# Kernel tuning notes

Measured on AMD Instinct MI355X. Metric: run time of the kernel, lower is better.

Reference implementation:

```python
import jax, jax.numpy as jnp
import numpy as np
from jax import lax

Q_SCALE = 128.0  # Q1.7 fixed point: 1 sign bit, 7 fractional bits


def quant_comp(x):
    """Q1.7 quantize (floor, clamp to [-128,127]) then force LSB=1 in the
    8-bit two's-complement pattern (equivalent to integer bitwise-or 1),
    then dequantize. Matches quantize_and_compensate_activation."""
    q = jnp.clip(jnp.floor(x * Q_SCALE), -128.0, 127.0).astype(jnp.int32)
    q = jnp.bitwise_or(q, 1)  # set LSB; in-range stays in [-127, 127]
    return q.astype(jnp.float32) / Q_SCALE


def conv2d(x, w, b, pad):
    y = lax.conv_general_dilated(
        x, w, window_strides=(1, 1), padding=[(pad, pad), (pad, pad)],
        dimension_numbers=("NCHW", "OIHW", "NCHW"))
    return y + b[None, :, None, None]


def maxpool2(x):
    return lax.reduce_window(x, -jnp.inf, lax.max,
                             (1, 1, 2, 2), (1, 1, 2, 2), "VALID")


def setup_inputs() -> dict:
    key = jax.random.key(0)
    ks = jax.random.split(key, 12)
    B = 16384

    def u(k, shape, fan_in):
        bound = 1.0 / np.sqrt(fan_in)
        return jax.random.uniform(k, shape, jnp.float32, -bound, bound)

    return {
        "x": jax.random.normal(ks[0], (B, 1, 28, 28), jnp.float32),
        "conv1_w": u(ks[1], (6, 1, 5, 5), 1 * 25),
        "conv1_b": u(ks[2], (6,), 1 * 25),
        "conv2_w": u(ks[3], (16, 6, 5, 5), 6 * 25),
        "conv2_b": u(ks[4], (16,), 6 * 25),
        "fc1_w": u(ks[5], (120, 400), 400),
        "fc1_b": u(ks[6], (120,), 400),
        "fc2_w": u(ks[7], (84, 120), 120),
        "fc2_b": u(ks[8], (84,), 120),
        "fc3_w": u(ks[9], (10, 84), 84),
        "fc3_b": u(ks[10], (10,), 84),
        "quant_act": 1,
    }


def reference(x, conv1_w, conv1_b, conv2_w, conv2_b,
              fc1_w, fc1_b, fc2_w, fc2_b, fc3_w, fc3_b, quant_act):
    q = bool(quant_act)
    if q:
        x = quant_comp(x)
    x = maxpool2(jax.nn.relu(conv2d(x, conv1_w, conv1_b, pad=2)))  # [B,6,14,14]
    if q:
        x = quant_comp(x)
    x = maxpool2(jax.nn.relu(conv2d(x, conv2_w, conv2_b, pad=0)))  # [B,16,5,5]
    if q:
        x = quant_comp(x)
    x = x.reshape(x.shape[0], -1)  # [B,400]
    x = jax.nn.relu(x @ fc1_w.T + fc1_b)
    if q:
        x = quant_comp(x)
    # dropout is identity in eval mode
    x = jax.nn.relu(x @ fc2_w.T + fc2_b)
    if q:
        x = quant_comp(x)
    return x @ fc3_w.T + fc3_b  # [B,10]
```

## Files before the change

kernel.cpp:

```cpp
#include <hip/hip_runtime.h>

#define Q_INV (1.0f / 128.0f)

__device__ __forceinline__ float quant_comp_f(float v) {
    float f = floorf(v * 128.0f);
    f = fminf(fmaxf(f, -128.0f), 127.0f);
    int qi = (int)f;
    qi |= 1;
    return (float)qi * Q_INV;
}

__device__ __forceinline__ float getf(const float4 v, const int c) {
    return c == 0 ? v.x : (c == 1 ? v.y : (c == 2 ? v.z : v.w));
}

__global__ __launch_bounds__(192) void conv_fused_kernel(
    const float* __restrict__ x,
    const float* __restrict__ c1w, const float* __restrict__ c1b,
    const float* __restrict__ c2w, const float* __restrict__ c2b,
    const int* __restrict__ qflag,
    float* __restrict__ act)
{
    __shared__ __align__(16) float shpool[3680];
    __shared__ float w1s[150];
    __shared__ float b1s[6];
    __shared__ float b2s[16];
    __shared__ __align__(16) float mid[6][14][20];

    float (*pin)[36] = reinterpret_cast<float(*)[36]>(shpool);

    const int t = threadIdx.x;
    const int img = blockIdx.x;
    const bool q = (qflag[0] != 0);

    for (int i = t; i < 1152; i += 192) shpool[i] = 0.0f;
    if (t < 150) w1s[t] = c1w[t];
    if (t < 6) b1s[t] = c1b[t];
    if (t < 16) b2s[t] = c2b[t];
    __syncthreads();

    const float* xi = x + (size_t)img * 784;
    for (int i = t; i < 784; i += 192) {
        float v = xi[i];
        if (q) v = quant_comp_f(v);
        pin[i / 28 + 2][i % 28 + 2] = v;
    }
    __syncthreads();

    float hmax1[14];
    if (t < 168) {
        const int c = t / 28, oh = t % 28;
        float acc[28];
        #pragma unroll
        for (int j = 0; j < 28; ++j) acc[j] = 0.0f;
        #pragma unroll
        for (int ky = 0; ky < 5; ++ky) {
            const float4* pr = reinterpret_cast<const float4*>(&pin[oh + ky][0]);
            float4 r4[8];
            #pragma unroll
            for (int j = 0; j < 8; ++j) r4[j] = pr[j];
            #pragma unroll
            for (int kx = 0; kx < 5; ++kx) {
                const float wv = w1s[c * 25 + ky * 5 + kx];
                #pragma unroll
                for (int ow = 0; ow < 28; ++ow) {
                    const int idx = ow + kx;
                    acc[ow] = fmaf(getf(r4[idx >> 2], idx & 3), wv, acc[ow]);
                }
            }
        }
        const float bb = b1s[c];
        #pragma unroll
        for (int j = 0; j < 14; ++j) {
            float v0 = acc[2*j] + bb;
            float v1 = acc[2*j + 1] + bb;
            hmax1[j] = fmaxf(v0, v1);
        }
    }
    __syncthreads();
    if (t < 168) {
        const int c = t / 28, oh = t % 28;
        #pragma unroll
        for (int j = 0; j < 14; ++j) shpool[(c * 28 + oh) * 17 + j] = hmax1[j];
    }
    __syncthreads();
    if (t < 84) {
        const int c = t / 14, ph = t % 14;
        #pragma unroll
        for (int j = 0; j < 14; ++j) {
            float m = fmaxf(shpool[(c * 28 + 2 * ph) * 17 + j],
                            shpool[(c * 28 + 2 * ph + 1) * 17 + j]);
            m = fmaxf(m, 0.0f);
            if (q) m = quant_comp_f(m);
            mid[c][ph][j] = m;
        }
    }
    __syncthreads();

    {
        const float4* src = reinterpret_cast<const float4*>(c2w);
        float4* dst = reinterpret_cast<float4*>(shpool);
        for (int i = t; i < 600; i += 192) dst[i] = src[i];
    }
    __syncthreads();

    const float* w2s = shpool;
    float* rowmax2 = shpool + 2400;

    float hmax2[5];
    if (t < 160) {
        const int c = t / 10, oh = t % 10;
        float acc[10];
        #pragma unroll
        for (int j = 0; j < 10; ++j) acc[j] = 0.0f;
        #pragma unroll
        for (int ky = 0; ky < 5; ++ky) {
            float4 rb4[6][4];
            #pragma unroll
            for (int ic = 0; ic < 6; ++ic) {
                const float4* mr = reinterpret_cast<const float4*>(&mid[ic][oh + ky][0]);
                #pragma unroll
                for (int j2 = 0; j2 < 4; ++j2) rb4[ic][j2] = mr[j2];
            }
            #pragma unroll
            for (int kx = 0; kx < 5; ++kx) {
                #pragma unroll
                for (int ic = 0; ic < 6; ++ic) {
                    const float wv = w2s[(c * 6 + ic) * 25 + ky * 5 + kx];
                    #pragma unroll
                    for (int ow = 0; ow < 10; ++ow) {
                        const int idx = ow + kx;
                        acc[ow] = fmaf(getf(rb4[ic][idx >> 2], idx & 3), wv, acc[ow]);
                    }
                }
            }
        }
        const float bb = b2s[c];
        #pragma unroll
        for (int j = 0; j < 5; ++j) {
            float v0 = acc[2*j] + bb;
            float v1 = acc[2*j + 1] + bb;
            hmax2[j] = fmaxf(v0, v1);
        }
    }
    if (t < 160) {
        const int c = t / 10, oh = t % 10;
        #pragma unroll
        for (int j = 0; j < 5; ++j) rowmax2[(c * 10 + oh) * 8 + j] = hmax2[j];
    }
    __syncthreads();
    if (t < 80) {
        const int c = t / 5, ph = t % 5;
        float* ao = act + (size_t)img * 400;
        #pragma unroll
        for (int j = 0; j < 5; ++j) {
            float m = fmaxf(rowmax2[(c * 10 + 2 * ph) * 8 + j],
                            rowmax2[(c * 10 + 2 * ph + 1) * 8 + j]);
            m = fmaxf(m, 0.0f);
            if (q) m = quant_comp_f(m);
            ao[c * 25 + ph * 5 + j] = m;
        }
    }
}

__global__ __launch_bounds__(256) void fc_fused_kernel(
    const float* __restrict__ act,
    const float* __restrict__ w1, const float* __restrict__ b1,
    const float* __restrict__ w2, const float* __restrict__ b2,
    const float* __restrict__ w3, const float* __restrict__ b3,
    const int* __restrict__ qflag,
    float* __restrict__ out, int B)
{
    __shared__ __align__(16) float wt[120][44];
    __shared__ __align__(16) float a0c[16][44];
    __shared__ __align__(16) float a1[16][124];
    __shared__ __align__(16) float a2[16][88];

    const int t = threadIdx.x;
    const bool q = (qflag[0] != 0);
    const int base = blockIdx.x * 16;
    const int im = t & 15;
    const int grp = t >> 4;

    float acc[8];
    #pragma unroll
    for (int j = 0; j < 8; ++j) acc[j] = 0.0f;

    for (int ch = 0; ch < 10; ++ch) {
        __syncthreads();
        for (int i = t; i < 1200; i += 256) {
            const int o = i / 10, s = i % 10;
            *reinterpret_cast<float4*>(&wt[o][s * 4]) =
                *reinterpret_cast<const float4*>(w1 + o * 400 + ch * 40 + s * 4);
        }
        for (int i = t; i < 640; i += 256) {
            const int imm = i / 40, k = i % 40;
            if (base + imm < B)
                a0c[imm][k] = act[(size_t)(base + imm) * 400 + ch * 40 + k];
        }
        __syncthreads();
        #pragma unroll
        for (int r = 0; r < 4; ++r) {
            const int o0 = r * 32 + 2 * grp;
            if (o0 < 120) {
                float s0 = acc[2*r], s1 = acc[2*r+1];
                #pragma unroll
                for (int kk = 0; kk < 10; ++kk) {
                    const float4 av = *reinterpret_cast<const float4*>(&a0c[im][kk*4]);
                    const float4 wa = *reinterpret_cast<const float4*>(&wt[o0][kk*4]);
                    const float4 wb = *reinterpret_cast<const float4*>(&wt[o0+1][kk*4]);
                    s0 = fmaf(av.x, wa.x, s0); s1 = fmaf(av.x, wb.x, s1);
                    s0 = fmaf(av.y, wa.y, s0); s1 = fmaf(av.y, wb.y, s1);
                    s0 = fmaf(av.z, wa.z, s0); s1 = fmaf(av.z, wb.z, s1);
                    s0 = fmaf(av.w, wa.w, s0); s1 = fmaf(av.w, wb.w, s1);
                }
                acc[2*r] = s0; acc[2*r+1] = s1;
            }
        }
    }
    #pragma unroll
    for (int r = 0; r < 4; ++r) {
        const int o0 = r * 32 + 2 * grp;
        if (o0 < 120) {
            float v0 = acc[2*r] + b1[o0];
            float v1 = acc[2*r+1] + b1[o0+1];
            v0 = fmaxf(v0, 0.0f); v1 = fmaxf(v1, 0.0f);
            a1[im][o0]   = q ? quant_comp_f(v0) : v0;
            a1[im][o0+1] = q ? quant_comp_f(v1) : v1;
        }
    }

    float bcc[6];
    #pragma unroll
    for (int j = 0; j < 6; ++j) bcc[j] = 0.0f;

    for (int ch = 0; ch < 3; ++ch) {
        __syncthreads();
        for (int i = t; i < 840; i += 256) {
            const int o = i / 10, s = i % 10;
            *reinterpret_cast<float4*>(&wt[o][s * 4]) =
                *reinterpret_cast<const float4*>(w2 + o * 120 + ch * 40 + s * 4);
        }
        __syncthreads();
        #pragma unroll
        for (int r = 0; r < 3; ++r) {
            const int o0 = r * 32 + 2 * grp;
            if (o0 < 84) {
                float s0 = bcc[2*r], s1 = bcc[2*r+1];
                #pragma unroll
                for (int kk = 0; kk < 10; ++kk) {
                    const float4 av = *reinterpret_cast<const float4*>(&a1[im][ch*40 + kk*4]);
                    const float4 wa = *reinterpret_cast<const float4*>(&wt[o0][kk*4]);
                    const float4 wb = *reinterpret_cast<const float4*>(&wt[o0+1][kk*4]);
                    s0 = fmaf(av.x, wa.x, s0); s1 = fmaf(av.x, wb.x, s1);
                    s0 = fmaf(av.y, wa.y, s0); s1 = fmaf(av.y, wb.y, s1);
                    s0 = fmaf(av.z, wa.z, s0); s1 = fmaf(av.z, wb.z, s1);
                    s0 = fmaf(av.w, wa.w, s0); s1 = fmaf(av.w, wb.w, s1);
                }
                bcc[2*r] = s0; bcc[2*r+1] = s1;
            }
        }
    }
    #pragma unroll
    for (int r = 0; r < 3; ++r) {
        const int o0 = r * 32 + 2 * grp;
        if (o0 < 84) {
            float v0 = bcc[2*r] + b2[o0];
            float v1 = bcc[2*r+1] + b2[o0+1];
            v0 = fmaxf(v0, 0.0f); v1 = fmaxf(v1, 0.0f);
            a2[im][o0]   = q ? quant_comp_f(v0) : v0;
            a2[im][o0+1] = q ? quant_comp_f(v1) : v1;
        }
    }

    __syncthreads();
    {
        float* wtf = &wt[0][0];
        for (int i = t; i < 210; i += 256)
            reinterpret_cast<float4*>(wtf)[i] =
                reinterpret_cast<const float4*>(w3)[i];
    }
    __syncthreads();
    {
        const int o0 = 2 * grp;
        if (o0 < 10) {
            const float* wtf = &wt[0][0];
            float s0 = 0.0f, s1 = 0.0f;
            #pragma unroll
            for (int kk = 0; kk < 21; ++kk) {
                const float4 av = *reinterpret_cast<const float4*>(&a2[im][kk*4]);
                const float4 wa = *reinterpret_cast<const float4*>(&wtf[o0*84 + kk*4]);
                const float4 wb = *reinterpret_cast<const float4*>(&wtf[(o0+1)*84 + kk*4]);
                s0 = fmaf(av.x, wa.x, s0); s1 = fmaf(av.x, wb.x, s1);
                s0 = fmaf(av.y, wa.y, s0); s1 = fmaf(av.y, wb.y, s1);
                s0 = fmaf(av.z, wa.z, s0); s1 = fmaf(av.z, wb.z, s1);
                s0 = fmaf(av.w, wa.w, s0); s1 = fmaf(av.w, wb.w, s1);
            }
            if (base + im < B) {
                out[(size_t)(base + im) * 10 + o0]     = s0 + b3[o0];
                out[(size_t)(base + im) * 10 + o0 + 1] = s1 + b3[o0 + 1];
            }
        }
    }
}

extern "C" void kernel_launch(void* const* d_in, const int* in_sizes, int n_in,
                              void* d_out, int out_size, void* d_ws, size_t ws_size,
                              hipStream_t stream) {
    const float* x     = (const float*)d_in[0];
    const float* c1w   = (const float*)d_in[1];
    const float* c1b   = (const float*)d_in[2];
    const float* c2w   = (const float*)d_in[3];
    const float* c2b   = (const float*)d_in[4];
    const float* fc1w  = (const float*)d_in[5];
    const float* fc1b  = (const float*)d_in[6];
    const float* fc2w  = (const float*)d_in[7];
    const float* fc2b  = (const float*)d_in[8];
    const float* fc3w  = (const float*)d_in[9];
    const float* fc3b  = (const float*)d_in[10];
    const int*   qflag = (const int*)d_in[11];
    float* out = (float*)d_out;

    const int B = in_sizes[0] / 784;
    float* act = (float*)d_ws;

    conv_fused_kernel<<<B, 192, 0, stream>>>(x, c1w, c1b, c2w, c2b, qflag, act);

    const int nblk = (B + 15) / 16;
    fc_fused_kernel<<<nblk, 256, 0, stream>>>(act, fc1w, fc1b, fc2w, fc2b,
                                              fc3w, fc3b, qflag, out, B);
}
```

Baseline: 324.1 us.

## Retile FC1/FC2 register blocking to 4 outputs x 2 images per thread

Changes the fc kernel's thread mapping so each thread computes 4 output neurons for 2 images instead of 2 outputs for 1 image. Weight rows are permuted into shared memory slots so each thread reads rows og, og+30 (or og+21), and so on. Activation chunk loads are vectorized to float4. The aim is more FMAs per shared-memory load and fewer LDS operations, at the cost of idle threads (og>=30 or og>=21) and a permuted weight-load index calculation.

```diff
diff --git a/kernel.cpp b/kernel.cpp
--- a/kernel.cpp
+++ b/kernel.cpp
@@ -179,97 +179,120 @@
     const int t = threadIdx.x;
     const bool q = (qflag[0] != 0);
     const int base = blockIdx.x * 16;
-    const int im = t & 15;
-    const int grp = t >> 4;
-
-    float acc[8];
+    const int og = t >> 3;
+    const int ig = t & 7;
+
+    float acc[4][2];
     #pragma unroll
-    for (int j = 0; j < 8; ++j) acc[j] = 0.0f;
+    for (int j = 0; j < 4; ++j) { acc[j][0] = 0.0f; acc[j][1] = 0.0f; }
 
     for (int ch = 0; ch < 10; ++ch) {
         __syncthreads();
         for (int i = t; i < 1200; i += 256) {
-            const int o = i / 10, s = i % 10;
-            *reinterpret_cast<float4*>(&wt[o][s * 4]) =
-                *reinterpret_cast<const float4*>(w1 + o * 400 + ch * 40 + s * 4);
-        }
-        for (int i = t; i < 640; i += 256) {
-            const int imm = i / 40, k = i % 40;
+            const int slot = i / 10, s = i % 10;
+            const int orig = ((slot % 30) << 2) + (slot / 30);
+            *reinterpret_cast<float4*>(&wt[slot][s * 4]) =
+                *reinterpret_cast<const float4*>(w1 + orig * 400 + ch * 40 + s * 4);
+        }
+        for (int i = t; i < 160; i += 256) {
+            const int imm = i / 10, s = i % 10;
             if (base + imm < B)
-                a0c[imm][k] = act[(size_t)(base + imm) * 400 + ch * 40 + k];
+                *reinterpret_cast<float4*>(&a0c[imm][s * 4]) =
+                    *reinterpret_cast<const float4*>(act + (size_t)(base + imm) * 400 + ch * 40 + s * 4);
         }
         __syncthreads();
-        #pragma unroll
-        for (int r = 0; r < 4; ++r) {
-            const int o0 = r * 32 + 2 * grp;
-            if (o0 < 120) {
-                float s0 = acc[2*r], s1 = acc[2*r+1];
-                #pragma unroll
-                for (int kk = 0; kk < 10; ++kk) {
-                    const float4 av = *reinterpret_cast<const float4*>(&a0c[im][kk*4]);
-                    const float4 wa = *reinterpret_cast<const float4*>(&wt[o0][kk*4]);
-                    const float4 wb = *reinterpret_cast<const float4*>(&wt[o0+1][kk*4]);
-                    s0 = fmaf(av.x, wa.x, s0); s1 = fmaf(av.x, wb.x, s1);
-                    s0 = fmaf(av.y, wa.y, s0); s1 = fmaf(av.y, wb.y, s1);
-                    s0 = fmaf(av.z, wa.z, s0); s1 = fmaf(av.z, wb.z, s1);
-                    s0 = fmaf(av.w, wa.w, s0); s1 = fmaf(av.w, wb.w, s1);
-                }
-                acc[2*r] = s0; acc[2*r+1] = s1;
-            }
-        }
-    }
+        if (og < 30) {
+            #pragma unroll
+            for (int kk = 0; kk < 10; ++kk) {
+                const float4 av0 = *reinterpret_cast<const float4*>(&a0c[2*ig][kk*4]);
+                const float4 av1 = *reinterpret_cast<const float4*>(&a0c[2*ig+1][kk*4]);
+                const float4 w0 = *reinterpret_cast<const float4*>(&wt[og][kk*4]);
+                const float4 wv1 = *reinterpret_cast<const float4*>(&wt[30+og][kk*4]);
+                const float4 wv2 = *reinterpret_cast<const float4*>(&wt[60+og][kk*4]);
+                const float4 wv3 = *reinterpret_cast<const float4*>(&wt[90+og][kk*4]);
+                acc[0][0]=fmaf(av0.x,w0.x,acc[0][0]);  acc[0][1]=fmaf(av1.x,w0.x,acc[0][1]);
+                acc[1][0]=fmaf(av0.x,wv1.x,acc[1][0]); acc[1][1]=fmaf(av1.x,wv1.x,acc[1][1]);
+                acc[2][0]=fmaf(av0.x,wv2.x,acc[2][0]); acc[2][1]=fmaf(av1.x,wv2.x,acc[2][1]);
+                acc[3][0]=fmaf(av0.x,wv3.x,acc[3][0]); acc[3][1]=fmaf(av1.x,wv3.x,acc[3][1]);
+                acc[0][0]=fmaf(av0.y,w0.y,acc[0][0]);  acc[0][1]=fmaf(av1.y,w0.y,acc[0][1]);
+                acc[1][0]=fmaf(av0.y,wv1.y,acc[1][0]); acc[1][1]=fmaf(av1.y,wv1.y,acc[1][1]);
+                acc[2][0]=fmaf(av0.y,wv2.y,acc[2][0]); acc[2][1]=fmaf(av1.y,wv2.y,acc[2][1]);
+                acc[3][0]=fmaf(av0.y,wv3.y,acc[3][0]); acc[3][1]=fmaf(av1.y,wv3.y,acc[3][1]);
+                acc[0][0]=fmaf(av0.z,w0.z,acc[0][0]);  acc[0][1]=fmaf(av1.z,w0.z,acc[0][1]);
+                acc[1][0]=fmaf(av0.z,wv1.z,acc[1][0]); acc[1][1]=fmaf(av1.z,wv1.z,acc[1][1]);
+                acc[2][0]=fmaf(av0.z,wv2.z,acc[2][0]); acc[2][1]=fmaf(av1.z,wv2.z,acc[2][1]);
+                acc[3][0]=fmaf(av0.z,wv3.z,acc[3][0]); acc[3][1]=fmaf(av1.z,wv3.z,acc[3][1]);
+                acc[0][0]=fmaf(av0.w,w0.w,acc[0][0]);  acc[0][1]=fmaf(av1.w,w0.w,acc[0][1]);
+                acc[1][0]=fmaf(av0.w,wv1.w,acc[1][0]); acc[1][1]=fmaf(av1.w,wv1.w,acc[1][1]);
+                acc[2][0]=fmaf(av0.w,wv2.w,acc[2][0]); acc[2][1]=fmaf(av1.w,wv2.w,acc[2][1]);
+                acc[3][0]=fmaf(av0.w,wv3.w,acc[3][0]); acc[3][1]=fmaf(av1.w,wv3.w,acc[3][1]);
+            }
+        }
+    }
+    if (og < 30) {
+        #pragma unroll
+        for (int j = 0; j < 4; ++j) {
+            const int o = og * 4 + j;
+            #pragma unroll
+            for (int i = 0; i < 2; ++i) {
+                float v = acc[j][i] + b1[o];
+                v = fmaxf(v, 0.0f);
+                a1[2*ig + i][o] = q ? quant_comp_f(v) : v;
+            }
+        }
+    }
+
+    float bcc[4][2];
     #pragma unroll
-    for (int r = 0; r < 4; ++r) {
-        const int o0 = r * 32 + 2 * grp;
-        if (o0 < 120) {
-            float v0 = acc[2*r] + b1[o0];
-            float v1 = acc[2*r+1] + b1[o0+1];
-            v0 = fmaxf(v0, 0.0f); v1 = fmaxf(v1, 0.0f);
-            a1[im][o0]   = q ? quant_comp_f(v0) : v0;
-            a1[im][o0+1] = q ? quant_comp_f(v1) : v1;
-        }
-    }
-
-    float bcc[6];
-    #pragma unroll
-    for (int j = 0; j < 6; ++j) bcc[j] = 0.0f;
+    for (int j = 0; j < 4; ++j) { bcc[j][0] = 0.0f; bcc[j][1] = 0.0f; }
 
     for (int ch = 0; ch < 3; ++ch) {
         __syncthreads();
         for (int i = t; i < 840; i += 256) {
-            const int o = i / 10, s = i % 10;
-            *reinterpret_cast<float4*>(&wt[o][s * 4]) =
-                *reinterpret_cast<const float4*>(w2 + o * 120 + ch * 40 + s * 4);
+            const int slot = i / 10, s = i % 10;
+            const int orig = ((slot % 21) << 2) + (slot / 21);
+            *reinterpret_cast<float4*>(&wt[slot][s * 4]) =
+                *reinterpret_cast<const float4*>(w2 + orig * 120 + ch * 40 + s * 4);
         }
         __syncthreads();
-        #pragma unroll
-        for (int r = 0; r < 3; ++r) {
-            const int o0 = r * 32 + 2 * grp;
-            if (o0 < 84) {
-                float s0 = bcc[2*r], s1 = bcc[2*r+1];
-                #pragma unroll
-                for (int kk = 0; kk < 10; ++kk) {
-                    const float4 av = *reinterpret_cast<const float4*>(&a1[im][ch*40 + kk*4]);
-                    const float4 wa = *reinterpret_cast<const float4*>(&wt[o0][kk*4]);
-                    const float4 wb = *reinterpret_cast<const float4*>(&wt[o0+1][kk*4]);
-                    s0 = fmaf(av.x, wa.x, s0); s1 = fmaf(av.x, wb.x, s1);
-                    s0 = fmaf(av.y, wa.y, s0); s1 = fmaf(av.y, wb.y, s1);
-                    s0 = fmaf(av.z, wa.z, s0); s1 = fmaf(av.z, wb.z, s1);
-                    s0 = fmaf(av.w, wa.w, s0); s1 = fmaf(av.w, wb.w, s1);
-                }
-                bcc[2*r] = s0; bcc[2*r+1] = s1;
-            }
-        }
-    }
-    #pragma unroll
-    for (int r = 0; r < 3; ++r) {
-        const int o0 = r * 32 + 2 * grp;
-        if (o0 < 84) {
-            float v0 = bcc[2*r] + b2[o0];
-            float v1 = bcc[2*r+1] + b2[o0+1];
-            v0 = fmaxf(v0, 0.0f); v1 = fmaxf(v1, 0.0f);
-            a2[im][o0]   = q ? quant_comp_f(v0) : v0;
-            a2[im][o0+1] = q ? quant_comp_f(v1) : v1;
+        if (og < 21) {
+            #pragma unroll
+            for (int kk = 0; kk < 10; ++kk) {
+                const float4 av0 = *reinterpret_cast<const float4*>(&a1[2*ig][ch*40 + kk*4]);
+                const float4 av1 = *reinterpret_cast<const float4*>(&a1[2*ig+1][ch*40 + kk*4]);
+                const float4 w0 = *reinterpret_cast<const float4*>(&wt[og][kk*4]);
+                const float4 wv1 = *reinterpret_cast<const float4*>(&wt[21+og][kk*4]);
+                const float4 wv2 = *reinterpret_cast<const float4*>(&wt[42+og][kk*4]);
+                const float4 wv3 = *reinterpret_cast<const float4*>(&wt[63+og][kk*4]);
+                bcc[0][0]=fmaf(av0.x,w0.x,bcc[0][0]);  bcc[0][1]=fmaf(av1.x,w0.x,bcc[0][1]);
+                bcc[1][0]=fmaf(av0.x,wv1.x,bcc[1][0]); bcc[1][1]=fmaf(av1.x,wv1.x,bcc[1][1]);
+                bcc[2][0]=fmaf(av0.x,wv2.x,bcc[2][0]); bcc[2][1]=fmaf(av1.x,wv2.x,bcc[2][1]);
+                bcc[3][0]=fmaf(av0.x,wv3.x,bcc[3][0]); bcc[3][1]=fmaf(av1.x,wv3.x,bcc[3][1]);
+                bcc[0][0]=fmaf(av0.y,w0.y,bcc[0][0]);  bcc[0][1]=fmaf(av1.y,w0.y,bcc[0][1]);
+                bcc[1][0]=fmaf(av0.y,wv1.y,bcc[1][0]); bcc[1][1]=fmaf(av1.y,wv1.y,bcc[1][1]);
+                bcc[2][0]=fmaf(av0.y,wv2.y,bcc[2][0]); bcc[2][1]=fmaf(av1.y,wv2.y,bcc[2][1]);
+                bcc[3][0]=fmaf(av0.y,wv3.y,bcc[3][0]); bcc[3][1]=fmaf(av1.y,wv3.y,bcc[3][1]);
+                bcc[0][0]=fmaf(av0.z,w0.z,bcc[0][0]);  bcc[0][1]=fmaf(av1.z,w0.z,bcc[0][1]);
+                bcc[1][0]=fmaf(av0.z,wv1.z,bcc[1][0]); bcc[1][1]=fmaf(av1.z,wv1.z,bcc[1][1]);
+                bcc[2][0]=fmaf(av0.z,wv2.z,bcc[2][0]); bcc[2][1]=fmaf(av1.z,wv2.z,bcc[2][1]);
+                bcc[3][0]=fmaf(av0.z,wv3.z,bcc[3][0]); bcc[3][1]=fmaf(av1.z,wv3.z,bcc[3][1]);
+                bcc[0][0]=fmaf(av0.w,w0.w,bcc[0][0]);  bcc[0][1]=fmaf(av1.w,w0.w,bcc[0][1]);
+                bcc[1][0]=fmaf(av0.w,wv1.w,bcc[1][0]); bcc[1][1]=fmaf(av1.w,wv1.w,bcc[1][1]);
+                bcc[2][0]=fmaf(av0.w,wv2.w,bcc[2][0]); bcc[2][1]=fmaf(av1.w,wv2.w,bcc[2][1]);
+                bcc[3][0]=fmaf(av0.w,wv3.w,bcc[3][0]); bcc[3][1]=fmaf(av1.w,wv3.w,bcc[3][1]);
+            }
+        }
+    }
+    if (og < 21) {
+        #pragma unroll
+        for (int j = 0; j < 4; ++j) {
+            const int o = og * 4 + j;
+            #pragma unroll
+            for (int i = 0; i < 2; ++i) {
+                float v = bcc[j][i] + b2[o];
+                v = fmaxf(v, 0.0f);
+                a2[2*ig + i][o] = q ? quant_comp_f(v) : v;
+            }
         }
     }
 
@@ -282,6 +305,8 @@
     }
     __syncthreads();
     {
+        const int grp = t >> 4;
+        const int im = t & 15;
         const int o0 = 2 * grp;
         if (o0 < 10) {
             const float* wtf = &wt[0][0];
```

Result: faster. 295.7 us (-8.8%).
